# Optimization experiments

Measured on AMD Instinct MI355X. Metric: run time of the kernel, lower is better.

## Reference

```python
import jax, jax.numpy as jnp
import numpy as np

N = 400000   # nodes; must equal E because the original code computes `out + x` with out per-edge
E = 400000   # edges
HID = 128
HEADS = 4
NEG_SLOPE = 0.01  # torch F.leaky_relu default


def setup_inputs() -> dict:
    key = jax.random.key(0)
    k1, k2, k3, k4 = jax.random.split(key, 4)
    x = jax.random.normal(k1, (N, HID), dtype=jnp.float32)
    edge_index = jax.random.randint(k2, (2, E), 0, N, dtype=jnp.int64)
    # xavier-uniform-ish scale for the attention parameter [1, heads, 2*hidden]
    lim_a = float(np.sqrt(6.0 / (1 + HEADS * 2 * HID)))
    attention = jax.random.uniform(k3, (1, HEADS, 2 * HID), jnp.float32, -lim_a, lim_a)
    lim_w = float(np.sqrt(1.0 / (HID * HEADS)))
    W = jax.random.uniform(k4, (HID, HID * HEADS), jnp.float32, -lim_w, lim_w)
    b = jnp.zeros((HID,), jnp.float32)
    return {"x": x, "edge_index": edge_index, "attention": attention, "W": W, "b": b}


def _scatter_softmax(s, seg, num_segments):
    # softmax over edges grouped by destination node index `seg` (axis 0)
    m = jax.lax.stop_gradient(jax.ops.segment_max(s, seg, num_segments=num_segments))
    ex = jnp.exp(s - m[seg])
    denom = jax.ops.segment_sum(ex, seg, num_segments=num_segments)
    return ex / denom[seg]


def reference(x, edge_index, attention, W, b):
    row, col = edge_index[0], edge_index[1]
    # [E, 2*HID] per-edge concatenated features
    ef = jnp.concatenate([x[row], x[col]], axis=-1)
    # per-head scores: (ef[:,None,:] * attention).sum(-1) -> [E, HEADS]
    scores = jnp.einsum('ef,hf->eh', ef, attention[0])
    scores = jax.nn.leaky_relu(scores, NEG_SLOPE)
    scores = jax.nn.softmax(scores, axis=1)      # softmax across heads (as in source)
    # dropout(p=0.1) -> identity in eval mode
    alpha = _scatter_softmax(scores, row, N)     # [E, HEADS] per-destination softmax
    # per-head weighted source features, concatenated over heads -> [E, HEADS*HID]
    feats = (alpha[:, :, None] * x[col][:, None, :]).reshape(E, HEADS * HID)
    out = feats @ W.T + b                        # Linear(hidden*heads -> hidden)
    return out + x
```

## Files before the change

kernel.cpp:

```cpp
#include <hip/hip_runtime.h>

#define NN 400000
#define NE 400000

typedef __attribute__((ext_vector_type(4))) float f32x4;
typedef __attribute__((ext_vector_type(8))) short s16x8;
typedef unsigned short ushort_t;

__device__ __forceinline__ ushort_t f2bf(float f) {
    union { float f; unsigned int u; } c;
    c.f = f;
    unsigned int u = c.u;
    u = u + 0x7fffu + ((u >> 16) & 1u);
    return (ushort_t)(u >> 16);
}
__device__ __forceinline__ float bf2f(ushort_t v) {
    union { unsigned int u; float f; } c;
    c.u = ((unsigned int)v) << 16;
    return c.f;
}

__global__ void k_detect(const int* __restrict__ ei_raw, int* __restrict__ flag) {
    if (threadIdx.x == 0 && blockIdx.x == 0) {
        int is64 = 1;
        for (int i = 0; i < 64; i++)
            if (ei_raw[2 * i + 1] != 0) { is64 = 0; break; }
        flag[0] = is64;
    }
}

__global__ void k_cvt_idx(const int* __restrict__ ei_raw, const int* __restrict__ flag,
                          int* __restrict__ ei32) {
    const int i = blockIdx.x * 256 + threadIdx.x;
    const int f = flag[0];
    ei32[i] = f ? ei_raw[2 * i] : ei_raw[i];
}

__global__ void k_wcvt(const float* __restrict__ W, ushort_t* __restrict__ wbf) {
    const int i = blockIdx.x * 256 + threadIdx.x;
    wbf[i] = f2bf(W[i]);
}

__global__ void k_uv_cvt(const float* __restrict__ x, const float* __restrict__ att,
                         ushort_t* __restrict__ xbf, float* __restrict__ uv) {
    const int lane = threadIdx.x & 63;
    const int wid = threadIdx.x >> 6;
    const int g = lane & 15;
    const int ns = lane >> 4;

    float areg[8][8];
#pragma unroll
    for (int h = 0; h < 4; h++) {
        const f32x4 fa = *(const f32x4*)(att + h * 256 + g * 8);
        const f32x4 fb = *(const f32x4*)(att + h * 256 + g * 8 + 4);
        const f32x4 ba = *(const f32x4*)(att + h * 256 + 128 + g * 8);
        const f32x4 bb = *(const f32x4*)(att + h * 256 + 128 + g * 8 + 4);
#pragma unroll
        for (int m = 0; m < 4; m++) {
            areg[h][m] = fa[m];     areg[h][4 + m] = fb[m];
            areg[4 + h][m] = ba[m]; areg[4 + h][4 + m] = bb[m];
        }
    }

    for (int tile = blockIdx.x; tile < NN / 32; tile += gridDim.x) {
        const int nb = tile * 32 + wid * 8 + ns;
#pragma unroll
        for (int t = 0; t < 2; t++) {
            const int n = nb + t * 4;
            const f32x4 xa = *(const f32x4*)(x + (size_t)n * 128 + g * 8);
            const f32x4 xb = *(const f32x4*)(x + (size_t)n * 128 + g * 8 + 4);
            s16x8 pk;
#pragma unroll
            for (int m = 0; m < 4; m++) { pk[m] = (short)f2bf(xa[m]); pk[4 + m] = (short)f2bf(xb[m]); }
            *(s16x8*)(xbf + (size_t)n * 128 + g * 8) = pk;
            float r[8];
#pragma unroll
            for (int v = 0; v < 8; v++) {
                float s = 0.f;
#pragma unroll
                for (int m = 0; m < 4; m++) s += xa[m] * areg[v][m];
#pragma unroll
                for (int m = 0; m < 4; m++) s += xb[m] * areg[v][4 + m];
                r[v] = s;
            }
#pragma unroll
            for (int mask = 1; mask <= 4; mask <<= 1)
#pragma unroll
                for (int v = 0; v < 8; v++) r[v] += __shfl_xor(r[v], mask, 64);
            const int gv = g & 7;
            float s = r[0];
#pragma unroll
            for (int v = 1; v < 8; v++) s = (gv == v) ? r[v] : s;
            s += __shfl_xor(s, 8, 64);
            if (g < 8) uv[(size_t)n * 8 + g] = s;
        }
    }
}

__global__ void k_edge(const int* __restrict__ ei, const float* __restrict__ uv,
                       float* __restrict__ p, float* __restrict__ denom) {
    const int e = blockIdx.x * 256 + threadIdx.x;
    if (e >= NE) return;
    const int row = ei[e];
    const int col = ei[NE + e];
    const f32x4 u = *(const f32x4*)(uv + (size_t)row * 8);
    const f32x4 v = *(const f32x4*)(uv + (size_t)col * 8 + 4);
    float s[4];
    float mx = -1e30f;
#pragma unroll
    for (int h = 0; h < 4; h++) {
        float t = u[h] + v[h];
        t = t > 0.f ? t : 0.01f * t;
        s[h] = t;
        mx = fmaxf(mx, t);
    }
    float ex[4], sum = 0.f;
#pragma unroll
    for (int h = 0; h < 4; h++) { ex[h] = __expf(s[h] - mx); sum += ex[h]; }
    const float inv = 1.f / sum;
    f32x4 pv;
#pragma unroll
    for (int h = 0; h < 4; h++) pv[h] = __expf(ex[h] * inv);
    *(f32x4*)(p + (size_t)e * 4) = pv;
#pragma unroll
    for (int h = 0; h < 4; h++) atomicAdd(denom + (size_t)row * 4 + h, pv[h]);
}

__global__ __launch_bounds__(1024, 4) void k_gemm(
    const ushort_t* __restrict__ xbf, const int* __restrict__ ei,
    const float* __restrict__ p, const float* __restrict__ denom,
    const ushort_t* __restrict__ wbf, const float* __restrict__ bias,
    float* __restrict__ out)
{
    __shared__ __align__(16) ushort_t Bsm[128 * 512];
    __shared__ __align__(16) ushort_t Asm[128 * 128];

    const int tid = threadIdx.x;
    const int lane = tid & 63;
    const int w = tid >> 6;
    const int eg = w & 3;
    const int cg = w >> 2;

    {
        const int icol = tid & 127, seg = tid >> 7;
        const ushort_t* src = wbf + icol * 512 + seg * 64;
#pragma unroll
        for (int m = 0; m < 8; m++) {
            const s16x8 v = *(const s16x8*)(src + m * 8);
            const int byte = icol * 1024 + ((seg * 128 + m * 16) ^ ((icol & 15) << 4));
            *(s16x8*)((char*)Bsm + byte) = v;
        }
    }
    float bias_r[2];
#pragma unroll
    for (int cbi = 0; cbi < 2; cbi++) bias_r[cbi] = bias[cg * 32 + cbi * 16 + (lane & 15)];

    const f32x4 zero = {0.f, 0.f, 0.f, 0.f};
    const int ntiles = NE / 128;

#pragma unroll 1
    for (int tile = blockIdx.x; tile < ntiles; tile += gridDim.x) {
        __syncthreads();
#pragma unroll
        for (int i = 0; i < 2; i++) {
            const int rr = w * 8 + i * 4 + (lane >> 4);
            const int col = ei[NE + tile * 128 + rr];
            const int c = (lane & 15) ^ (rr & 15);
            const ushort_t* src = xbf + (size_t)col * 128 + c * 8;
            __builtin_amdgcn_global_load_lds(
                (const __attribute__((address_space(1))) unsigned int*)src,
                (__attribute__((address_space(3))) unsigned int*)((char*)Asm + w * 2048 + i * 1024),
                16, 0, 0);
        }
        f32x4 alp;
        {
            const int e = tile * 128 + eg * 32 + (lane & 31);
            const int row = ei[e];
            const f32x4 pv = *(const f32x4*)(p + (size_t)e * 4);
            const f32x4 dv = *(const f32x4*)(denom + (size_t)row * 4);
            alp = pv / dv;
        }
        f32x4 av[4][2];
#pragma unroll
        for (int h = 0; h < 4; h++)
#pragma unroll
            for (int eb = 0; eb < 2; eb++)
#pragma unroll
                for (int r = 0; r < 4; r++)
                    av[h][eb][r] = __shfl(alp[h], eb * 16 + (lane >> 4) * 4 + r, 64);
        __syncthreads();

        s16x8 af[2][4];
#pragma unroll
        for (int eb = 0; eb < 2; eb++) {
            const int rr = eg * 32 + eb * 16 + (lane & 15);
#pragma unroll
            for (int ks = 0; ks < 4; ks++) {
                const int byte = rr * 256 + ((ks * 64 + (lane >> 4) * 16) ^ ((rr & 15) << 4));
                af[eb][ks] = *(const s16x8*)((const char*)Asm + byte);
            }
        }

        f32x4 fin[2][2];
#pragma unroll
        for (int eb = 0; eb < 2; eb++)
#pragma unroll
            for (int cbi = 0; cbi < 2; cbi++) fin[eb][cbi] = zero;

#pragma unroll
        for (int h = 0; h < 4; h++) {
            s16x8 bfr[2][4];
#pragma unroll
            for (int cbi = 0; cbi < 2; cbi++) {
                const int icol = cg * 32 + cbi * 16 + (lane & 15);
#pragma unroll
                for (int ks = 0; ks < 4; ks++) {
                    const int byte = icol * 1024 +
                        ((h * 256 + ks * 64 + (lane >> 4) * 16) ^ ((icol & 15) << 4));
                    bfr[cbi][ks] = *(const s16x8*)((const char*)Bsm + byte);
                }
            }
#pragma unroll
            for (int eb = 0; eb < 2; eb++)
#pragma unroll
                for (int cbi = 0; cbi < 2; cbi++) {
                    f32x4 a = __builtin_amdgcn_mfma_f32_16x16x32_bf16(af[eb][0], bfr[cbi][0], zero, 0, 0, 0);
#pragma unroll
                    for (int ks = 1; ks < 4; ks++)
                        a = __builtin_amdgcn_mfma_f32_16x16x32_bf16(af[eb][ks], bfr[cbi][ks], a, 0, 0, 0);
                    fin[eb][cbi] += av[h][eb] * a;
                }
        }
#pragma unroll
        for (int eb = 0; eb < 2; eb++)
#pragma unroll
            for (int cbi = 0; cbi < 2; cbi++) {
                const int icol = cg * 32 + cbi * 16 + (lane & 15);
#pragma unroll
                for (int r = 0; r < 4; r++) {
                    const int e = tile * 128 + eg * 32 + eb * 16 + (lane >> 4) * 4 + r;
                    const size_t off = (size_t)e * 128 + icol;
                    out[off] = fin[eb][cbi][r] + bias_r[cbi] + bf2f(xbf[off]);
                }
            }
    }
}

extern "C" void kernel_launch(void* const* d_in, const int* in_sizes, int n_in,
                              void* d_out, int out_size, void* d_ws, size_t ws_size,
                              hipStream_t stream) {
    const float* x      = (const float*)d_in[0];
    const int*   ei_raw = (const int*)d_in[1];
    const float* att    = (const float*)d_in[2];
    const float* W      = (const float*)d_in[3];
    const float* b      = (const float*)d_in[4];
    float* out = (float*)d_out;

    char* ws = (char*)d_ws;
    float*    uv      = (float*)(ws);
    float*    p       = (float*)(ws + 12800000);
    float*    denom   = (float*)(ws + 19200000);
    ushort_t* wbf     = (ushort_t*)(ws + 32000000);
    int*      flag    = (int*)(ws + 32200000);
    int*      ei32    = (int*)(ws + 32200064);
    ushort_t* xbf     = (ushort_t*)(ws + 35400192);

    hipMemsetAsync(denom, 0, (size_t)NN * 4 * sizeof(float), stream);
    k_detect<<<1, 64, 0, stream>>>(ei_raw, flag);
    k_cvt_idx<<<2 * NE / 256, 256, 0, stream>>>(ei_raw, flag, ei32);
    k_wcvt<<<256, 256, 0, stream>>>(W, wbf);
    k_uv_cvt<<<2048, 256, 0, stream>>>(x, att, xbf, uv);
    k_edge<<<(NE + 255) / 256, 256, 0, stream>>>(ei32, uv, p, denom);
    k_gemm<<<256, 1024, 0, stream>>>(xbf, ei32, p, denom, wbf, b, out);
}
```

Baseline: 301.2 us.

## Double-buffer gathered A tiles and precompute alpha in separate kernel

Splits the per-edge alpha normalisation (p / denom[row]) into its own kernel, so the GEMM kernel reads one precomputed vector per edge instead of doing a dependent gather. The GEMM tile shrinks from 128 to 64 edges and the gathered source-feature tile is double-buffered in LDS, so the next tile's gather is issued before the current tile's MFMA work. Waves are remapped so each handles 16 output columns instead of 32. This adds one kernel launch and an extra E×4 float round trip, and halves the reuse of B-fragment loads per tile.

```diff
diff --git a/kernel.cpp b/kernel.cpp
--- a/kernel.cpp
+++ b/kernel.cpp
@@ -126,20 +126,29 @@
     for (int h = 0; h < 4; h++) atomicAdd(denom + (size_t)row * 4 + h, pv[h]);
 }
 
+__global__ void k_alpha(const int* __restrict__ ei, const float* __restrict__ p,
+                        const float* __restrict__ denom, float* __restrict__ alpha4) {
+    const int e = blockIdx.x * 256 + threadIdx.x;
+    if (e >= NE) return;
+    const int row = ei[e];
+    const f32x4 pv = *(const f32x4*)(p + (size_t)e * 4);
+    const f32x4 dv = *(const f32x4*)(denom + (size_t)row * 4);
+    *(f32x4*)(alpha4 + (size_t)e * 4) = pv / dv;
+}
+
 __global__ __launch_bounds__(1024, 4) void k_gemm(
     const ushort_t* __restrict__ xbf, const int* __restrict__ ei,
-    const float* __restrict__ p, const float* __restrict__ denom,
-    const ushort_t* __restrict__ wbf, const float* __restrict__ bias,
-    float* __restrict__ out)
+    const float* __restrict__ alpha4, const ushort_t* __restrict__ wbf,
+    const float* __restrict__ bias, float* __restrict__ out)
 {
     __shared__ __align__(16) ushort_t Bsm[128 * 512];
-    __shared__ __align__(16) ushort_t Asm[128 * 128];
+    __shared__ __align__(16) ushort_t Asm[2][64 * 128];
 
     const int tid = threadIdx.x;
     const int lane = tid & 63;
     const int w = tid >> 6;
-    const int eg = w & 3;
-    const int cg = w >> 2;
+    const int eg = w & 1;
+    const int cg = w >> 1;
 
     {
         const int icol = tid & 127, seg = tid >> 7;
@@ -151,44 +160,35 @@
             *(s16x8*)((char*)Bsm + byte) = v;
         }
     }
-    float bias_r[2];
-#pragma unroll
-    for (int cbi = 0; cbi < 2; cbi++) bias_r[cbi] = bias[cg * 32 + cbi * 16 + (lane & 15)];
+    const int icol = cg * 16 + (lane & 15);
+    const float bias_r = bias[icol];
 
     const f32x4 zero = {0.f, 0.f, 0.f, 0.f};
-    const int ntiles = NE / 128;
+    const int ntiles = NE / 64;
+    const int stride = gridDim.x;
+
+    auto STAGE = [&](int tt, int b) {
+        const int rr = w * 4 + (lane >> 4);
+        const int col = ei[NE + tt * 64 + rr];
+        const int c = (lane & 15) ^ (rr & 15);
+        const ushort_t* src = xbf + (size_t)col * 128 + c * 8;
+        __builtin_amdgcn_global_load_lds(
+            (const __attribute__((address_space(1))) unsigned int*)src,
+            (__attribute__((address_space(3))) unsigned int*)((char*)Asm[b] + w * 1024),
+            16, 0, 0);
+    };
+
+    int t = blockIdx.x;
+    int cur = 0;
+    if (t < ntiles) STAGE(t, 0);
 
 #pragma unroll 1
-    for (int tile = blockIdx.x; tile < ntiles; tile += gridDim.x) {
+    for (; t < ntiles; t += stride) {
         __syncthreads();
-#pragma unroll
-        for (int i = 0; i < 2; i++) {
-            const int rr = w * 8 + i * 4 + (lane >> 4);
-            const int col = ei[NE + tile * 128 + rr];
-            const int c = (lane & 15) ^ (rr & 15);
-            const ushort_t* src = xbf + (size_t)col * 128 + c * 8;
-            __builtin_amdgcn_global_load_lds(
-                (const __attribute__((address_space(1))) unsigned int*)src,
-                (__attribute__((address_space(3))) unsigned int*)((char*)Asm + w * 2048 + i * 1024),
-                16, 0, 0);
-        }
-        f32x4 alp;
-        {
-            const int e = tile * 128 + eg * 32 + (lane & 31);
-            const int row = ei[e];
-            const f32x4 pv = *(const f32x4*)(p + (size_t)e * 4);
-            const f32x4 dv = *(const f32x4*)(denom + (size_t)row * 4);
-            alp = pv / dv;
-        }
-        f32x4 av[4][2];
-#pragma unroll
-        for (int h = 0; h < 4; h++)
-#pragma unroll
-            for (int eb = 0; eb < 2; eb++)
-#pragma unroll
-                for (int r = 0; r < 4; r++)
-                    av[h][eb][r] = __shfl(alp[h], eb * 16 + (lane >> 4) * 4 + r, 64);
-        __syncthreads();
+        const int tn = t + stride;
+        if (tn < ntiles) STAGE(tn, cur ^ 1);
+
+        const f32x4 alp = *(const f32x4*)(alpha4 + (size_t)(t * 64 + eg * 32 + (lane & 31)) * 4);
 
         s16x8 af[2][4];
 #pragma unroll
@@ -197,52 +197,45 @@
 #pragma unroll
             for (int ks = 0; ks < 4; ks++) {
                 const int byte = rr * 256 + ((ks * 64 + (lane >> 4) * 16) ^ ((rr & 15) << 4));
-                af[eb][ks] = *(const s16x8*)((const char*)Asm + byte);
-            }
-        }
-
-        f32x4 fin[2][2];
-#pragma unroll
-        for (int eb = 0; eb < 2; eb++)
-#pragma unroll
-            for (int cbi = 0; cbi < 2; cbi++) fin[eb][cbi] = zero;
+                af[eb][ks] = *(const s16x8*)((const char*)Asm[cur] + byte);
+            }
+        }
+
+        f32x4 fin[2];
+        fin[0] = zero; fin[1] = zero;
 
 #pragma unroll
         for (int h = 0; h < 4; h++) {
-            s16x8 bfr[2][4];
-#pragma unroll
-            for (int cbi = 0; cbi < 2; cbi++) {
-                const int icol = cg * 32 + cbi * 16 + (lane & 15);
-#pragma unroll
-                for (int ks = 0; ks < 4; ks++) {
-                    const int byte = icol * 1024 +
-                        ((h * 256 + ks * 64 + (lane >> 4) * 16) ^ ((icol & 15) << 4));
-                    bfr[cbi][ks] = *(const s16x8*)((const char*)Bsm + byte);
-                }
-            }
-#pragma unroll
-            for (int eb = 0; eb < 2; eb++)
-#pragma unroll
-                for (int cbi = 0; cbi < 2; cbi++) {
-                    f32x4 a = __builtin_amdgcn_mfma_f32_16x16x32_bf16(af[eb][0], bfr[cbi][0], zero, 0, 0, 0);
-#pragma unroll
-                    for (int ks = 1; ks < 4; ks++)
-                        a = __builtin_amdgcn_mfma_f32_16x16x32_bf16(af[eb][ks], bfr[cbi][ks], a, 0, 0, 0);
-                    fin[eb][cbi] += av[h][eb] * a;
-                }
-        }
-#pragma unroll
-        for (int eb = 0; eb < 2; eb++)
-#pragma unroll
-            for (int cbi = 0; cbi < 2; cbi++) {
-                const int icol = cg * 32 + cbi * 16 + (lane & 15);
-#pragma unroll
-                for (int r = 0; r < 4; r++) {
-                    const int e = tile * 128 + eg * 32 + eb * 16 + (lane >> 4) * 4 + r;
-                    const size_t off = (size_t)e * 128 + icol;
-                    out[off] = fin[eb][cbi][r] + bias_r[cbi] + bf2f(xbf[off]);
-                }
-            }
+            s16x8 bfr[4];
+#pragma unroll
+            for (int ks = 0; ks < 4; ks++) {
+                const int byte = icol * 1024 +
+                    ((h * 256 + ks * 64 + (lane >> 4) * 16) ^ ((icol & 15) << 4));
+                bfr[ks] = *(const s16x8*)((const char*)Bsm + byte);
+            }
+#pragma unroll
+            for (int eb = 0; eb < 2; eb++) {
+                f32x4 a = __builtin_amdgcn_mfma_f32_16x16x32_bf16(af[eb][0], bfr[0], zero, 0, 0, 0);
+#pragma unroll
+                for (int ks = 1; ks < 4; ks++)
+                    a = __builtin_amdgcn_mfma_f32_16x16x32_bf16(af[eb][ks], bfr[ks], a, 0, 0, 0);
+                f32x4 av;
+#pragma unroll
+                for (int r = 0; r < 4; r++)
+                    av[r] = __shfl(alp[h], eb * 16 + (lane >> 4) * 4 + r, 64);
+                fin[eb] += av * a;
+            }
+        }
+#pragma unroll
+        for (int eb = 0; eb < 2; eb++) {
+#pragma unroll
+            for (int r = 0; r < 4; r++) {
+                const int e = t * 64 + eg * 32 + eb * 16 + (lane >> 4) * 4 + r;
+                const size_t off = (size_t)e * 128 + icol;
+                out[off] = fin[eb][r] + bias_r + bf2f(xbf[off]);
+            }
+        }
+        cur ^= 1;
     }
 }
 
@@ -260,6 +253,7 @@
     float*    uv      = (float*)(ws);
     float*    p       = (float*)(ws + 12800000);
     float*    denom   = (float*)(ws + 19200000);
+    float*    alpha4  = (float*)(ws + 25600000);
     ushort_t* wbf     = (ushort_t*)(ws + 32000000);
     int*      flag    = (int*)(ws + 32200000);
     int*      ei32    = (int*)(ws + 32200064);
@@ -271,5 +265,6 @@
     k_wcvt<<<256, 256, 0, stream>>>(W, wbf);
     k_uv_cvt<<<2048, 256, 0, stream>>>(x, att, xbf, uv);
     k_edge<<<(NE + 255) / 256, 256, 0, stream>>>(ei32, uv, p, denom);
-    k_gemm<<<256, 1024, 0, stream>>>(xbf, ei32, p, denom, wbf, b, out);
-}
+    k_alpha<<<(NE + 255) / 256, 256, 0, stream>>>(ei32, p, denom, alpha4);
+    k_gemm<<<256, 1024, 0, stream>>>(xbf, ei32, alpha4, wbf, b, out);
+}
```

Result: faster. 287.5 us (-4.5%).
